# Performance work log

Measured on AMD Instinct MI355X. Metric: run time of the kernel, lower is better.

## Reference

```python
import jax, jax.numpy as jnp
import numpy as np

B, C, H, W = 2, 4, 32, 256   # batch, num_classes (class 0 = background), range-image H x W
N = H * W                    # candidate points per (batch, class)
RADIUS = 3.0
KM_ITERS = 1
COORD_SCALE = 60.0           # spread lidar x/y so radius-3 NMS is non-trivial


def setup_inputs() -> dict:
    key = jax.random.key(0)
    k1, k2 = jax.random.split(key)
    segmented_channels = jax.random.normal(k1, (B, C, H, W), dtype=jnp.float32)
    lidar = jax.random.normal(k2, (B, 2, H, W), dtype=jnp.float32) * COORD_SCALE
    return {"segmented_channels": segmented_channels, "lidar": lidar}


def _radius_nms(points, mask, radius):
    # Greedy radius NMS in index order: keep point i iff no earlier kept point
    # lies within `radius`. Masked-out points are never kept (keep init = mask).
    n = points.shape[0]
    idx = jnp.arange(n)
    r2 = radius * radius

    def step(keep, i):
        d2 = jnp.sum((points - points[i]) ** 2, axis=-1)       # [N]
        suppress = keep & (d2 < r2) & (idx > i) & keep[i]
        return keep & ~suppress, None

    keep, _ = jax.lax.scan(step, mask, idx)
    return keep


def _kmeans(points, mask, keep, iters):
    # Centers initialized at the NMS-kept points (same index space as points).
    # Each valid class point is assigned to nearest valid center; centers move
    # to the mean of their assigned points.
    n = points.shape[0]
    centers = points
    w = mask.astype(points.dtype)
    BIG = jnp.asarray(1e30, points.dtype)
    for _ in range(iters):
        d2 = jnp.sum((points[:, None, :] - centers[None, :, :]) ** 2, axis=-1)  # [N,N]
        d2 = jnp.where(keep[None, :], d2, BIG)
        assign = jnp.argmin(d2, axis=1)                         # [N]
        sums = jax.ops.segment_sum(points * w[:, None], assign, num_segments=n)
        cnt = jax.ops.segment_sum(w, assign, num_segments=n)
        upd = sums / jnp.maximum(cnt, 1.0)[:, None]
        centers = jnp.where((keep & (cnt > 0))[:, None], upd, centers)
    return centers * keep[:, None].astype(points.dtype)


def reference(segmented_channels, lidar):
    ind = jnp.argmax(segmented_channels, axis=1)                # [B,H,W] class id per cell
    pts = jnp.stack([lidar[:, 0], lidar[:, 1]], axis=-1).reshape(B, N, 2)
    # boolean class masks for foreground classes 1..C-1
    cls_mask = jnp.stack([ind == c for c in range(1, C)], axis=1).reshape(B, C - 1, N)
    pts_all = jnp.broadcast_to(pts[:, None], (B, C - 1, N, 2)).reshape(B * (C - 1), N, 2)
    mask_all = cls_mask.reshape(B * (C - 1), N)

    def per_bc(args):
        p, m = args
        keep = _radius_nms(p, m, RADIUS)
        centers = _kmeans(p, m, keep, KM_ITERS)
        return centers, keep

    centers, keep = jax.lax.map(per_bc, (pts_all, mask_all))
    # centers: padded [B, C-1, N, 2]; keep marks which rows are real detections
    return centers.reshape(B, C - 1, N, 2), keep.reshape(B, C - 1, N)
```

## Files before the change

### kernel.cpp

```cpp
#include <hip/hip_runtime.h>

#define NPTS 8192
#define BCLS 4
#define NP   6
#define R2   9.0f
#define RAD  3.0f
#define GRD  128
#define NCELL (GRD*GRD)
#define PCAP 2048
#define LDSK 2048
#define CAP  4096
#define KBLK 64
#define KTHR 256

#define ST_U 0u
#define ST_A 1u
#define ST_D 2u


__global__ __launch_bounds__(KTHR) void k_front(
    const float* __restrict__ seg, const float* __restrict__ lidar,
    float* __restrict__ xs, float* __restrict__ ys,
    unsigned int* __restrict__ ns, unsigned int* __restrict__ counts,
    float* __restrict__ out)
{
    const int tid = threadIdx.x, lane = tid & 63;
    const int idx = blockIdx.x * KTHR + tid;
    const int b = idx >> 13, n = idx & 8191;

    __shared__ float ex[KTHR], ey[KTHR];
    __shared__ unsigned short en[KTHR];
    __shared__ unsigned int cnt6[6], off6[6], pos6[6];

    if (tid < 6) cnt6[tid] = 0;
    __syncthreads();

    const float* segb = seg + (size_t)b * BCLS * NPTS + n;
    float bv = segb[0];
    int bc = 0;
    #pragma unroll
    for (int c = 1; c < BCLS; ++c) {
        float v = segb[(size_t)c * NPTS];
        if (v > bv) { bv = v; bc = c; }
    }
    const float x = lidar[(size_t)b * 2 * NPTS + n];
    const float y = lidar[(size_t)b * 2 * NPTS + NPTS + n];
    const int p = (bc > 0) ? (b * 3 + bc - 1) : -1;

    #pragma unroll
    for (int q = 0; q < 6; ++q) {
        unsigned long long bal = __ballot(p == q);
        if (lane == 0 && bal) atomicAdd(&cnt6[q], (unsigned int)__popcll(bal));
    }
    __syncthreads();
    if (tid == 0) {
        unsigned int a = 0;
        #pragma unroll
        for (int q = 0; q < 6; ++q) { off6[q] = a; pos6[q] = a; a += cnt6[q]; }
    }
    __syncthreads();
    #pragma unroll
    for (int q = 0; q < 6; ++q) {
        unsigned long long bal = __ballot(p == q);
        if (bal) {
            int ldr = __builtin_ctzll(bal);
            unsigned int wb = 0;
            if (lane == ldr) wb = atomicAdd(&pos6[q], (unsigned int)__popcll(bal));
            wb = __shfl(wb, ldr, 64);
            if (p == q) {
                unsigned int s = wb + (unsigned int)__popcll(bal & ((1ull << lane) - 1ull));
                ex[s] = x; ey[s] = y; en[s] = (unsigned short)n;
            }
        }
    }
    __syncthreads();
    {
        const unsigned int total = off6[5] + cnt6[5];
        const int gbase = blockIdx.x * KTHR;
        for (int k = tid; k < (int)total; k += KTHR) {
            xs[gbase + k] = ex[k];
            ys[gbase + k] = ey[k];
            ns[gbase + k] = (unsigned int)en[k];
        }
        if (tid < 6) counts[blockIdx.x * 6 + tid] = cnt6[tid];
    }
    {
        float4* o4 = (float4*)out;
        for (int k = idx; k < 36864; k += KBLK * KTHR)
            o4[k] = make_float4(0.f, 0.f, 0.f, 0.f);
    }
}

__global__ __launch_bounds__(1024) void k_nms(
    const float* __restrict__ xs, const float* __restrict__ ys,
    const unsigned int* __restrict__ ns, const unsigned int* __restrict__ counts,
    float* __restrict__ out)
{
    const int p = blockIdx.x;
    const int tid = threadIdx.x, lane = tid & 63, wv = tid >> 6;
    const int base = p * NPTS;

    __shared__ float2 sps[CAP];
    __shared__ unsigned int cmb[CAP];
    __shared__ unsigned int cellpack[NCELL];
    __shared__ unsigned short plist[2][PCAP];
    __shared__ float ksx[LDSK], ksy[LDSK], kcn[LDSK];
    __shared__ int pcnt[2];
    __shared__ unsigned long long ballots[64];
    __shared__ unsigned int base64[64];
    __shared__ unsigned int wtot[16];
    __shared__ float redbuf[4][16];
    __shared__ unsigned int csrc[KBLK], cdst[KBLK];
    __shared__ float sbminx, sbminy, scell;
    __shared__ int sM, sK;

    float* ok = out + (size_t)2 * NP * NPTS + base;

    for (int k = tid; k < CAP; k += 1024) cmb[k] = ST_U;
    for (int k = tid; k < NCELL; k += 1024) cellpack[k] = 0u;
    for (int k = tid; k < LDSK; k += 1024) { ksx[k] = 0.f; ksy[k] = 0.f; kcn[k] = 0.f; }
    if (tid == 0) { pcnt[0] = 0; pcnt[1] = 0; }

    if (wv == 0) {
        unsigned int c6[6];
        #pragma unroll
        for (int q = 0; q < 6; ++q) c6[q] = counts[lane * 6 + q];
        unsigned int within = 0;
        for (int q = 0; q < p; ++q) within += c6[q];
        unsigned int len = c6[p];
        unsigned int v = len;
        for (int d = 1; d < 64; d <<= 1) {
            unsigned int u = __shfl_up(v, d, 64);
            if (lane >= d) v += u;
        }
        csrc[lane] = lane * KTHR + within;
        cdst[lane] = v - len;
        if (lane == 63) sM = (int)(v < CAP ? v : CAP);
    }
    __syncthreads();
    const int M = sM;

    float xq[4], yq[4];
    unsigned int nq[4];
    int liq[4];
    {
        float mnx = 3e38f, mxx = -3e38f, mny = 3e38f, mxy = -3e38f;
        #pragma unroll
        for (int q = 0; q < 4; ++q) {
            int li = q * 1024 + tid;
            liq[q] = li;
            if (li < M) {
                int lo = 0, hi = KBLK - 1;
                #pragma unroll
                for (int s = 0; s < 6; ++s) {
                    int mid = (lo + hi + 1) >> 1;
                    if (cdst[mid] <= (unsigned int)li) lo = mid; else hi = mid - 1;
                }
                int si = csrc[lo] + (li - cdst[lo]);
                float x = xs[si], y = ys[si];
                xq[q] = x; yq[q] = y; nq[q] = ns[si];
                mnx = fminf(mnx, x); mxx = fmaxf(mxx, x);
                mny = fminf(mny, y); mxy = fmaxf(mxy, y);
            }
        }
        for (int d = 32; d; d >>= 1) {
            mnx = fminf(mnx, __shfl_xor(mnx, d, 64));
            mxx = fmaxf(mxx, __shfl_xor(mxx, d, 64));
            mny = fminf(mny, __shfl_xor(mny, d, 64));
            mxy = fmaxf(mxy, __shfl_xor(mxy, d, 64));
        }
        if (lane == 0) { redbuf[0][wv] = mnx; redbuf[1][wv] = mxx;
                         redbuf[2][wv] = mny; redbuf[3][wv] = mxy; }
    }
    __syncthreads();
    if (tid == 0) {
        float a = redbuf[0][0], b2 = redbuf[1][0], c = redbuf[2][0], d = redbuf[3][0];
        for (int q = 1; q < 16; ++q) {
            a = fminf(a, redbuf[0][q]); b2 = fmaxf(b2, redbuf[1][q]);
            c = fminf(c, redbuf[2][q]); d = fmaxf(d, redbuf[3][q]);
        }
        sbminx = a; sbminy = c;
        scell = fmaxf(2.0f * RAD, fmaxf(b2 - a, d - c) / 127.0f);
    }
    __syncthreads();
    const float bminx = sbminx, bminy = sbminy, inv = 1.0f / scell;

    int cellq[4];
    #pragma unroll
    for (int q = 0; q < 4; ++q) {
        if (liq[q] < M) {
            int ix = min(GRD - 1, max(0, (int)((xq[q] - bminx) * inv)));
            int iy = min(GRD - 1, max(0, (int)((yq[q] - bminy) * inv)));
            cellq[q] = iy * GRD + ix;
            atomicAdd(&cellpack[cellq[q]], 1u);
        } else cellq[q] = -1;
    }
    __syncthreads();
    {
        unsigned int c16[16], t16 = 0;
        #pragma unroll
        for (int q = 0; q < 16; ++q) { c16[q] = cellpack[tid * 16 + q]; t16 += c16[q]; }
        unsigned int v = t16;
        for (int d = 1; d < 64; d <<= 1) {
            unsigned int u = __shfl_up(v, d, 64);
            if (lane >= d) v += u;
        }
        if (lane == 63) wtot[wv] = v;
        __syncthreads();
        if (tid == 0) {
            unsigned int acc = 0;
            for (int q = 0; q < 16; ++q) { unsigned int t = wtot[q]; wtot[q] = acc; acc += t; }
        }
        __syncthreads();
        unsigned int excl = wtot[wv] + v - t16;
        #pragma unroll
        for (int q = 0; q < 16; ++q) { cellpack[tid * 16 + q] = excl << 16; excl += c16[q]; }
    }
    __syncthreads();
    #pragma unroll
    for (int q = 0; q < 4; ++q) {
        if (cellq[q] >= 0) {
            unsigned int old = atomicAdd(&cellpack[cellq[q]], 1u);
            unsigned int pos = (old >> 16) + (old & 0xffffu);
            sps[pos] = make_float2(xq[q], yq[q]);
            cmb[pos] = (nq[q] << 2) | ST_U;
        }
    }
    __syncthreads();

    #define ROW_FLAGS(CY, CX0, CX1, NI, ME, DEAD, UNDEC)                          \
    {                                                                             \
        unsigned int wa = cellpack[(CY) * GRD + (CX0)];                           \
        unsigned int wb = cellpack[(CY) * GRD + (CX1)];                           \
        unsigned int f0 = wa >> 16, f1 = (wb >> 16) + (wb & 0xffffu);             \
        for (unsigned int f = f0; f < f1; ++f) {                                  \
            unsigned int wf = cmb[f];                                             \
            float2 q = sps[f];                                                    \
            float dx = __fsub_rn((ME).x, q.x), dy = __fsub_rn((ME).y, q.y);       \
            float d2 = __fadd_rn(__fmul_rn(dx, dx), __fmul_rn(dy, dy));           \
            bool in = (d2 < R2) & ((int)(wf >> 2) < (NI));                        \
            DEAD  |= in & ((wf & 3u) == ST_A);                                    \
            UNDEC |= in & ((wf & 3u) == ST_U);                                    \
        }                                                                         \
    }
    #define SCAN_FLAGS(NI, ME, DEAD, UNDEC)                                       \
    {                                                                             \
        int cx0 = max(0, (int)(((ME).x - RAD - bminx) * inv));                    \
        int cx1 = min(GRD - 1, (int)(((ME).x + RAD - bminx) * inv));              \
        int cy0 = max(0, (int)(((ME).y - RAD - bminy) * inv));                    \
        int cy1 = min(GRD - 1, (int)(((ME).y + RAD - bminy) * inv));              \
        DEAD = false; UNDEC = false;                                              \
        ROW_FLAGS(cy0, cx0, cx1, NI, ME, DEAD, UNDEC);                            \
        if (cy1 > cy0) ROW_FLAGS(cy1, cx0, cx1, NI, ME, DEAD, UNDEC);             \
    }

    for (int e = tid; e < M; e += 1024) {
        unsigned int w = cmb[e];
        int ni = (int)(w >> 2);
        float2 me = sps[e];
        bool dead, undec;
        SCAN_FLAGS(ni, me, dead, undec);
        if (dead) cmb[e] = (w & ~3u) | ST_D;
        else if (!undec) cmb[e] = (w & ~3u) | ST_A;
        bool pendf = !dead && undec;
        unsigned long long act = __ballot(true);
        unsigned long long bal = __ballot(pendf);
        int leader = __builtin_ctzll(act);
        int cnt = __popcll(bal);
        int wbase = 0;
        if (lane == leader && cnt) wbase = atomicAdd(&pcnt[0], cnt);
        wbase = __shfl(wbase, leader, 64);
        if (pendf) {
            int pos = wbase + __popcll(bal & ((1ull << lane) - 1ull));
            if (pos < PCAP) plist[0][pos] = (unsigned short)e;
        }
    }

    int cur = 0;
    for (int round = 0; round < NPTS; ++round) {
        __syncthreads();
        int pc = pcnt[cur];
        if (pc == 0) break;
        if (pc > PCAP) {
            for (;;) {
                bool any = false;
                __syncthreads();
                for (int e = tid; e < M; e += 1024) {
                    unsigned int w = cmb[e];
                    if ((w & 3u) != ST_U) continue;
                    int ni = (int)(w >> 2);
                    float2 me = sps[e];
                    bool dead, undec;
                    SCAN_FLAGS(ni, me, dead, undec);
                    if (dead) cmb[e] = (w & ~3u) | ST_D;
                    else if (!undec) cmb[e] = (w & ~3u) | ST_A;
                    else any = true;
                }
                if (__syncthreads_count(any) == 0) break;
            }
            break;
        }
        if (tid == 0) pcnt[cur ^ 1] = 0;
        __syncthreads();
        for (int idx = tid; idx < pc; idx += 1024) {
            int e = plist[cur][idx];
            unsigned int w = cmb[e];
            int ni = (int)(w >> 2);
            float2 me = sps[e];
            bool dead, undec;
            SCAN_FLAGS(ni, me, dead, undec);
            if (dead) cmb[e] = (w & ~3u) | ST_D;
            else if (!undec) cmb[e] = (w & ~3u) | ST_A;
            bool pendf = !dead && undec;
            unsigned long long act = __ballot(true);
            unsigned long long bal = __ballot(pendf);
            int leader = __builtin_ctzll(act);
            int cnt = __popcll(bal);
            int wbase = 0;
            if (lane == leader && cnt) wbase = atomicAdd(&pcnt[cur ^ 1], cnt);
            wbase = __shfl(wbase, leader, 64);
            if (pendf) {
                int pos = wbase + __popcll(bal & ((1ull << lane) - 1ull));
                if (pos < PCAP) plist[cur ^ 1][pos] = (unsigned short)e;
            }
        }
        cur ^= 1;
    }
    __syncthreads();

    for (int k = 0; k < 4; ++k) {
        int e = (k << 10) + tid;
        unsigned long long bal = __ballot((cmb[e] & 3u) == ST_A);
        if (lane == 0) ballots[(k << 4) + wv] = bal;
    }
    __syncthreads();
    if (wv == 0) {
        unsigned int s = (unsigned int)__popcll(ballots[lane]);
        unsigned int v = s;
        for (int d = 1; d < 64; d <<= 1) {
            unsigned int u = __shfl_up(v, d, 64);
            if (lane >= d) v += u;
        }
        base64[lane] = v - s;
        if (lane == 63) sK = (int)v;
    }
    __syncthreads();
    #define KRANK(E) ((int)base64[(E) >> 6] +                                     \
                      __popcll(ballots[(E) >> 6] & ((1ull << ((E) & 63)) - 1ull)))

    #define ROW_ARGMIN(CY, CX0, CX1, ME, BD, BE, BN)                              \
    {                                                                             \
        unsigned int wa = cellpack[(CY) * GRD + (CX0)];                           \
        unsigned int wb = cellpack[(CY) * GRD + (CX1)];                           \
        unsigned int f0 = wa >> 16, f1 = (wb >> 16) + (wb & 0xffffu);             \
        for (unsigned int f = f0; f < f1; ++f) {                                  \
            unsigned int wf = cmb[f];                                             \
            float2 q = sps[f];                                                    \
            float dx = __fsub_rn((ME).x, q.x), dy = __fsub_rn((ME).y, q.y);       \
            float d2 = __fadd_rn(__fmul_rn(dx, dx), __fmul_rn(dy, dy));           \
            int nf = (int)(wf >> 2);                                              \
            bool better = ((wf & 3u) == ST_A) &                                   \
                          ((d2 < BD) | ((d2 == BD) & (nf < BN)));                 \
            BD = better ? d2 : BD;                                                \
            BE = better ? (int)f : BE;                                            \
            BN = better ? nf : BN;                                                \
        }                                                                         \
    }
    const int npass = (sK + LDSK - 1) / LDSK;
    for (int pass = 0; pass < npass; ++pass) {
        const int rb = pass * LDSK;
        if (pass) {
            __syncthreads();
            for (int k = tid; k < LDSK; k += 1024) { ksx[k] = 0.f; ksy[k] = 0.f; kcn[k] = 0.f; }
        }
        __syncthreads();
        for (int e = tid; e < M; e += 1024) {
            unsigned int w = cmb[e];
            float2 me = sps[e];
            int be;
            if ((w & 3u) == ST_A) {
                be = e;
            } else {
                int cx0 = max(0, (int)((me.x - RAD - bminx) * inv));
                int cx1 = min(GRD - 1, (int)((me.x + RAD - bminx) * inv));
                int cy0 = max(0, (int)((me.y - RAD - bminy) * inv));
                int cy1 = min(GRD - 1, (int)((me.y + RAD - bminy) * inv));
                float bd = 3e38f;
                be = -1;
                int bn = 1 << 30;
                ROW_ARGMIN(cy0, cx0, cx1, me, bd, be, bn);
                if (cy1 > cy0) ROW_ARGMIN(cy1, cx0, cx1, me, bd, be, bn);
                if (be < 0) continue;
            }
            int r = KRANK(be) - rb;
            if (r >= 0 && r < LDSK) {
                atomicAdd(&ksx[r], me.x);
                atomicAdd(&ksy[r], me.y);
                atomicAdd(&kcn[r], 1.0f);
            }
        }
        __syncthreads();
        for (int e = tid; e < M; e += 1024) {
            unsigned int w = cmb[e];
            if ((w & 3u) != ST_A) continue;
            int r = KRANK(e) - rb;
            if (r < 0 || r >= LDSK) continue;
            int n = (int)(w >> 2);
            float sx = ksx[r], sy = ksy[r], c = kcn[r];
            out[2 * (base + n)]     = sx / c;
            out[2 * (base + n) + 1] = sy / c;
            ok[n] = 1.0f;
        }
    }
}

extern "C" void kernel_launch(void* const* d_in, const int* in_sizes, int n_in,
                              void* d_out, int out_size, void* d_ws, size_t ws_size,
                              hipStream_t stream) {
    const float* seg   = (const float*)d_in[0];
    const float* lidar = (const float*)d_in[1];
    float* out = (float*)d_out;

    float* xs = (float*)d_ws;
    float* ys = xs + KBLK * KTHR;
    unsigned int* ns = (unsigned int*)(ys + KBLK * KTHR);
    unsigned int* counts = ns + KBLK * KTHR;

    k_front<<<KBLK, KTHR, 0, stream>>>(seg, lidar, xs, ys, ns, counts, out);
    k_nms<<<NP, 1024, 0, stream>>>(xs, ys, ns, counts, out);
}
```

Before: 101.7 us.

## Split k-means assignment into separate multi-block kernels via global workspace

```diff
diff --git a/kernel.cpp b/kernel.cpp
--- a/kernel.cpp
+++ b/kernel.cpp
@@ -8,10 +8,12 @@
 #define GRD  128
 #define NCELL (GRD*GRD)
 #define PCAP 2048
-#define LDSK 2048
 #define CAP  4096
 #define KBLK 64
 #define KTHR 256
+#define NSL  8
+#define WBLK (NP*NSL)
+#define WTHR 256
 
 #define ST_U 0u
 #define ST_A 1u
@@ -22,7 +24,7 @@
     const float* __restrict__ seg, const float* __restrict__ lidar,
     float* __restrict__ xs, float* __restrict__ ys,
     unsigned int* __restrict__ ns, unsigned int* __restrict__ counts,
-    float* __restrict__ out)
+    float* __restrict__ ksum, float* __restrict__ out)
 {
     const int tid = threadIdx.x, lane = tid & 63;
     const int idx = blockIdx.x * KTHR + tid;
@@ -88,23 +90,27 @@
         float4* o4 = (float4*)out;
         for (int k = idx; k < 36864; k += KBLK * KTHR)
             o4[k] = make_float4(0.f, 0.f, 0.f, 0.f);
+        float4* s4 = (float4*)ksum;
+        for (int k = idx; k < 18432; k += KBLK * KTHR)
+            s4[k] = make_float4(0.f, 0.f, 0.f, 0.f);
     }
 }
 
-__global__ __launch_bounds__(1024) void k_nms(
+__global__ __launch_bounds__(1024) void k_mid(
     const float* __restrict__ xs, const float* __restrict__ ys,
     const unsigned int* __restrict__ ns, const unsigned int* __restrict__ counts,
-    float* __restrict__ out)
+    float2* __restrict__ sps_g, unsigned int* __restrict__ cmb_g,
+    unsigned int* __restrict__ cellpack_g, float* __restrict__ bbox_g,
+    int* __restrict__ M_g,
+    unsigned long long* __restrict__ ballots_g, unsigned int* __restrict__ base_g)
 {
     const int p = blockIdx.x;
     const int tid = threadIdx.x, lane = tid & 63, wv = tid >> 6;
-    const int base = p * NPTS;
 
     __shared__ float2 sps[CAP];
     __shared__ unsigned int cmb[CAP];
     __shared__ unsigned int cellpack[NCELL];
     __shared__ unsigned short plist[2][PCAP];
-    __shared__ float ksx[LDSK], ksy[LDSK], kcn[LDSK];
     __shared__ int pcnt[2];
     __shared__ unsigned long long ballots[64];
     __shared__ unsigned int base64[64];
@@ -112,13 +118,10 @@
     __shared__ float redbuf[4][16];
     __shared__ unsigned int csrc[KBLK], cdst[KBLK];
     __shared__ float sbminx, sbminy, scell;
-    __shared__ int sM, sK;
-
-    float* ok = out + (size_t)2 * NP * NPTS + base;
+    __shared__ int sM;
 
     for (int k = tid; k < CAP; k += 1024) cmb[k] = ST_U;
     for (int k = tid; k < NCELL; k += 1024) cellpack[k] = 0u;
-    for (int k = tid; k < LDSK; k += 1024) { ksx[k] = 0.f; ksy[k] = 0.f; kcn[k] = 0.f; }
     if (tid == 0) { pcnt[0] = 0; pcnt[1] = 0; }
 
     if (wv == 0) {
@@ -227,6 +230,15 @@
         }
     }
     __syncthreads();
+
+    const int pb = p * CAP;
+    for (int k = tid; k < CAP; k += 1024) sps_g[pb + k] = sps[k];
+    for (int k = tid; k < NCELL; k += 1024) cellpack_g[p * NCELL + k] = cellpack[k];
+    if (tid == 0) {
+        bbox_g[p * 4 + 0] = bminx; bbox_g[p * 4 + 1] = bminy;
+        bbox_g[p * 4 + 2] = inv;
+        M_g[p] = M;
+    }
 
     #define ROW_FLAGS(CY, CX0, CX1, NI, ME, DEAD, UNDEC)                          \
     {                                                                             \
@@ -342,20 +354,41 @@
             if (lane >= d) v += u;
         }
         base64[lane] = v - s;
-        if (lane == 63) sK = (int)v;
-    }
-    __syncthreads();
-    #define KRANK(E) ((int)base64[(E) >> 6] +                                     \
-                      __popcll(ballots[(E) >> 6] & ((1ull << ((E) & 63)) - 1ull)))
-
-    #define ROW_ARGMIN(CY, CX0, CX1, ME, BD, BE, BN)                              \
+    }
+    __syncthreads();
+    for (int k = tid; k < CAP; k += 1024) cmb_g[pb + k] = cmb[k];
+    if (tid < 64) { ballots_g[(p << 6) + tid] = ballots[tid]; base_g[(p << 6) + tid] = base64[tid]; }
+}
+
+#define KRANK_G(P, E) ((int)base_g[((P) << 6) + ((E) >> 6)] +                     \
+    __popcll(ballots_g[((P) << 6) + ((E) >> 6)] & ((1ull << ((E) & 63)) - 1ull)))
+
+__global__ __launch_bounds__(WTHR) void k_assign(
+    const float2* __restrict__ sps_g, const unsigned int* __restrict__ cmb_g,
+    const unsigned int* __restrict__ cellpack_g, const float* __restrict__ bbox_g,
+    const int* __restrict__ M_g,
+    const unsigned long long* __restrict__ ballots_g, const unsigned int* __restrict__ base_g,
+    float* __restrict__ ksx, float* __restrict__ ksy, float* __restrict__ kcn)
+{
+    const int p = blockIdx.x / NSL, s = blockIdx.x % NSL;
+    const int tid = threadIdx.x;
+    const int M = M_g[p];
+    const float bminx = bbox_g[p * 4], bminy = bbox_g[p * 4 + 1], inv = bbox_g[p * 4 + 2];
+    const float2* sp = sps_g + p * CAP;
+    const unsigned int* cm = cmb_g + p * CAP;
+    const unsigned int* cp = cellpack_g + p * NCELL;
+
+    const int chunk = (M + NSL - 1) / NSL;
+    const int e0 = s * chunk, e1 = min(M, e0 + chunk);
+
+    #define G_ROW_ARGMIN(CY, CX0, CX1, ME, BD, BE, BN)                            \
     {                                                                             \
-        unsigned int wa = cellpack[(CY) * GRD + (CX0)];                           \
-        unsigned int wb = cellpack[(CY) * GRD + (CX1)];                           \
+        unsigned int wa = cp[(CY) * GRD + (CX0)];                                 \
+        unsigned int wb = cp[(CY) * GRD + (CX1)];                                 \
         unsigned int f0 = wa >> 16, f1 = (wb >> 16) + (wb & 0xffffu);             \
         for (unsigned int f = f0; f < f1; ++f) {                                  \
-            unsigned int wf = cmb[f];                                             \
-            float2 q = sps[f];                                                    \
+            unsigned int wf = cm[f];                                              \
+            float2 q = sp[f];                                                     \
             float dx = __fsub_rn((ME).x, q.x), dy = __fsub_rn((ME).y, q.y);       \
             float d2 = __fadd_rn(__fmul_rn(dx, dx), __fmul_rn(dy, dy));           \
             int nf = (int)(wf >> 2);                                              \
@@ -366,51 +399,56 @@
             BN = better ? nf : BN;                                                \
         }                                                                         \
     }
-    const int npass = (sK + LDSK - 1) / LDSK;
-    for (int pass = 0; pass < npass; ++pass) {
-        const int rb = pass * LDSK;
-        if (pass) {
-            __syncthreads();
-            for (int k = tid; k < LDSK; k += 1024) { ksx[k] = 0.f; ksy[k] = 0.f; kcn[k] = 0.f; }
-        }
-        __syncthreads();
-        for (int e = tid; e < M; e += 1024) {
-            unsigned int w = cmb[e];
-            float2 me = sps[e];
-            int be;
-            if ((w & 3u) == ST_A) {
-                be = e;
-            } else {
-                int cx0 = max(0, (int)((me.x - RAD - bminx) * inv));
-                int cx1 = min(GRD - 1, (int)((me.x + RAD - bminx) * inv));
-                int cy0 = max(0, (int)((me.y - RAD - bminy) * inv));
-                int cy1 = min(GRD - 1, (int)((me.y + RAD - bminy) * inv));
-                float bd = 3e38f;
-                be = -1;
-                int bn = 1 << 30;
-                ROW_ARGMIN(cy0, cx0, cx1, me, bd, be, bn);
-                if (cy1 > cy0) ROW_ARGMIN(cy1, cx0, cx1, me, bd, be, bn);
-                if (be < 0) continue;
-            }
-            int r = KRANK(be) - rb;
-            if (r >= 0 && r < LDSK) {
-                atomicAdd(&ksx[r], me.x);
-                atomicAdd(&ksy[r], me.y);
-                atomicAdd(&kcn[r], 1.0f);
-            }
-        }
-        __syncthreads();
-        for (int e = tid; e < M; e += 1024) {
-            unsigned int w = cmb[e];
-            if ((w & 3u) != ST_A) continue;
-            int r = KRANK(e) - rb;
-            if (r < 0 || r >= LDSK) continue;
-            int n = (int)(w >> 2);
-            float sx = ksx[r], sy = ksy[r], c = kcn[r];
-            out[2 * (base + n)]     = sx / c;
-            out[2 * (base + n) + 1] = sy / c;
-            ok[n] = 1.0f;
-        }
+    for (int e = e0 + tid; e < e1; e += WTHR) {
+        unsigned int w = cm[e];
+        float2 me = sp[e];
+        int be;
+        if ((w & 3u) == ST_A) {
+            be = e;
+        } else {
+            int cx0 = max(0, (int)((me.x - RAD - bminx) * inv));
+            int cx1 = min(GRD - 1, (int)((me.x + RAD - bminx) * inv));
+            int cy0 = max(0, (int)((me.y - RAD - bminy) * inv));
+            int cy1 = min(GRD - 1, (int)((me.y + RAD - bminy) * inv));
+            float bd = 3e38f;
+            be = -1;
+            int bn = 1 << 30;
+            G_ROW_ARGMIN(cy0, cx0, cx1, me, bd, be, bn);
+            if (cy1 > cy0) G_ROW_ARGMIN(cy1, cx0, cx1, me, bd, be, bn);
+            if (be < 0) continue;
+        }
+        int r = KRANK_G(p, be);
+        atomicAdd(&ksx[p * CAP + r], me.x);
+        atomicAdd(&ksy[p * CAP + r], me.y);
+        atomicAdd(&kcn[p * CAP + r], 1.0f);
+    }
+}
+
+__global__ __launch_bounds__(WTHR) void k_out(
+    const unsigned int* __restrict__ cmb_g, const int* __restrict__ M_g,
+    const unsigned long long* __restrict__ ballots_g, const unsigned int* __restrict__ base_g,
+    const float* __restrict__ ksx, const float* __restrict__ ksy,
+    const float* __restrict__ kcn, float* __restrict__ out)
+{
+    const int p = blockIdx.x / NSL, s = blockIdx.x % NSL;
+    const int tid = threadIdx.x;
+    const int M = M_g[p];
+    const unsigned int* cm = cmb_g + p * CAP;
+    const int base = p * NPTS;
+    float* ok = out + (size_t)2 * NP * NPTS + base;
+
+    const int chunk = (M + NSL - 1) / NSL;
+    const int e0 = s * chunk, e1 = min(M, e0 + chunk);
+
+    for (int e = e0 + tid; e < e1; e += WTHR) {
+        unsigned int w = cm[e];
+        if ((w & 3u) != ST_A) continue;
+        int n = (int)(w >> 2);
+        int r = KRANK_G(p, e);
+        float c = kcn[p * CAP + r];
+        out[2 * (base + n)]     = ksx[p * CAP + r] / c;
+        out[2 * (base + n) + 1] = ksy[p * CAP + r] / c;
+        ok[n] = 1.0f;
     }
 }
 
@@ -420,12 +458,27 @@
     const float* seg   = (const float*)d_in[0];
     const float* lidar = (const float*)d_in[1];
     float* out = (float*)d_out;
-
-    float* xs = (float*)d_ws;
-    float* ys = xs + KBLK * KTHR;
-    unsigned int* ns = (unsigned int*)(ys + KBLK * KTHR);
-    unsigned int* counts = ns + KBLK * KTHR;
-
-    k_front<<<KBLK, KTHR, 0, stream>>>(seg, lidar, xs, ys, ns, counts, out);
-    k_nms<<<NP, 1024, 0, stream>>>(xs, ys, ns, counts, out);
+    float* wsf = (float*)d_ws;
+
+    float* xs = wsf;
+    float* ys = wsf + 16384;
+    unsigned int* ns = (unsigned int*)(wsf + 32768);
+    unsigned int* counts = (unsigned int*)(wsf + 49152);
+    float2* sps_g = (float2*)(wsf + 49536);
+    unsigned int* cmb_g = (unsigned int*)(wsf + 98688);
+    unsigned int* cellpack_g = (unsigned int*)(wsf + 123264);
+    float* bbox_g = wsf + 221568;
+    int* M_g = (int*)(wsf + 221592);
+    unsigned long long* ballots_g = (unsigned long long*)(wsf + 221600);
+    unsigned int* base_g = (unsigned int*)(wsf + 222368);
+    float* ksx = wsf + 222752;
+    float* ksy = wsf + 247328;
+    float* kcn = wsf + 271904;
+
+    k_front <<<KBLK, KTHR, 0, stream>>>(seg, lidar, xs, ys, ns, counts, ksx, out);
+    k_mid   <<<NP, 1024, 0, stream>>>(xs, ys, ns, counts, sps_g, cmb_g, cellpack_g,
+                                      bbox_g, M_g, ballots_g, base_g);
+    k_assign<<<WBLK, WTHR, 0, stream>>>(sps_g, cmb_g, cellpack_g, bbox_g, M_g,
+                                        ballots_g, base_g, ksx, ksy, kcn);
+    k_out   <<<WBLK, WTHR, 0, stream>>>(cmb_g, M_g, ballots_g, base_g, ksx, ksy, kcn, out);
 }
```

Result: no change. 101.1 us, median of 2 (-0.6%).
